# Optimization experiments

Hardware: AMD Instinct MI355X
Metric: run time of the kernel (lower is better)

## Reference

```python
import math
import jax, jax.numpy as jnp
import numpy as np

B, SQ, SK, D, H = 4, 2048, 2048, 1024, 16
HD = D // H  # 64


def setup_inputs() -> dict:
    key = jax.random.key(0)
    k1, k2, k3, k4, k5 = jax.random.split(key, 5)
    scale = 1.0 / math.sqrt(D)
    return {
        "hidden_states": jax.random.normal(k1, (B, SQ, D), dtype=jnp.float32),
        "encoder_hidden_states": jax.random.normal(k2, (B, SK, D), dtype=jnp.float32),
        "Wq": jax.random.normal(k3, (D, D), dtype=jnp.float32) * scale,
        "Wk": jax.random.normal(k4, (D, D), dtype=jnp.float32) * scale,
        "Wv": jax.random.normal(k5, (D, D), dtype=jnp.float32) * scale,
    }


def reference(hidden_states, encoder_hidden_states, Wq, Wk, Wv):
    # Linear (bias=False): y = x @ W^T, then split heads -> [B, H, S, HD]
    def split_heads(x, S):
        return x.reshape(B, S, H, HD).transpose(0, 2, 1, 3)

    q = split_heads(hidden_states @ Wq.T, SQ)
    k = split_heads(encoder_hidden_states @ Wk.T, SK)
    v = split_heads(encoder_hidden_states @ Wv.T, SK)

    scores = jnp.einsum("bhqd,bhkd->bhqk", q, k) / math.sqrt(HD)
    probs = jax.nn.softmax(scores, axis=-1)  # no mask, dropout p=0
    ctx = jnp.einsum("bhqk,bhkd->bhqd", probs, v)
    # merge heads -> [B, SQ, D]
    return ctx.transpose(0, 2, 1, 3).reshape(B, SQ, D)
```

## Files before the change

kernel.cpp:

```cpp
#include <hip/hip_runtime.h>
#include <hip/hip_bf16.h>

typedef unsigned short u16;
typedef unsigned int u32;
typedef __attribute__((ext_vector_type(8))) short bf16x8;
typedef __attribute__((ext_vector_type(4))) float f32x4;

#define MFMA32(a, b, c) __builtin_amdgcn_mfma_f32_16x16x32_bf16(a, b, c, 0, 0, 0)

__device__ __forceinline__ float fexp2(float x) { return __builtin_amdgcn_exp2f(x); }

__device__ __forceinline__ u16 f2bf(float f) {
  u32 u = __float_as_uint(f);
  u += 0x7fffu + ((u >> 16) & 1u);
  return (u16)(u >> 16);
}
__device__ __forceinline__ u32 pack2rn(float a, float b) {
  return (u32)f2bf(a) | ((u32)f2bf(b) << 16);
}
__device__ __forceinline__ bf16x8 cvt8(const float4 a, const float4 b) {
  union { bf16x8 v; u32 p[4]; } r;
  r.p[0] = pack2rn(a.x, a.y); r.p[1] = pack2rn(a.z, a.w);
  r.p[2] = pack2rn(b.x, b.y); r.p[3] = pack2rn(b.z, b.w);
  return r.v;
}

__device__ __forceinline__ u32 cvtpk(float lo, float hi) {
  u32 r;
  asm("v_cvt_pk_bf16_f32 %0, %1, %2" : "=v"(r) : "v"(lo), "v"(hi));
  return r;
}
__device__ __forceinline__ void pl32swap(u32& a, u32& b) {
  asm("v_permlane32_swap_b32 %0, %1" : "+v"(a), "+v"(b));
}
__device__ __forceinline__ void pl16swap(u32& a, u32& b) {
  asm("v_permlane16_swap_b32 %0, %1" : "+v"(a), "+v"(b));
}

__device__ __forceinline__ void async_copy16(const void* g, void* l) {
  __builtin_amdgcn_global_load_lds(
      (const __attribute__((address_space(1))) unsigned int*)g,
      (__attribute__((address_space(3))) unsigned int*)l, 16, 0, 0);
}

__global__ __launch_bounds__(256) void cvt_bf16(
    const float* __restrict__ s0, const float* __restrict__ s1,
    const float* __restrict__ s2, const float* __restrict__ s3,
    const float* __restrict__ s4,
    u16* __restrict__ d0, u16* __restrict__ d1, u16* __restrict__ d2,
    u16* __restrict__ d3, u16* __restrict__ d4) {
  const int z = blockIdx.z;
  const float* s = (z == 0) ? s0 : (z == 1) ? s1 : (z == 2) ? s2 : (z == 3) ? s3 : s4;
  u16* d = (z == 0) ? d0 : (z == 1) ? d1 : (z == 2) ? d2 : (z == 3) ? d3 : d4;
  const int n8 = ((z < 2) ? (8192 * 1024) : (1024 * 1024)) / 8;
  const int stride = gridDim.x * 256;
  for (int i = blockIdx.x * 256 + threadIdx.x; i < n8; i += stride) {
    const float4 a = *(const float4*)(s + (size_t)i * 8);
    const float4 b = *(const float4*)(s + (size_t)i * 8 + 4);
    *(bf16x8*)(d + (size_t)i * 8) = cvt8(a, b);
  }
}

__global__ __launch_bounds__(256) void proj_gemm_bf(
    const u16* __restrict__ hb, const u16* __restrict__ eb,
    const u16* __restrict__ wb,
    u16* __restrict__ qb, u16* __restrict__ kb, u16* __restrict__ vt) {
  const int z = blockIdx.z;
  const u16* Ag = (z == 0) ? hb : eb;
  const u16* Bg = wb + (size_t)z * 1024 * 1024;
  const int m0 = blockIdx.y * 128;
  const int n0 = blockIdx.x * 128;
  __shared__ __attribute__((aligned(16))) u16 Al[128 * 32];
  __shared__ __attribute__((aligned(16))) u16 Bl[128 * 32];
  const int tid = threadIdx.x;
  const int w = tid >> 6, lane = tid & 63;
  const int wm = w >> 1, wn = w & 1;
  const int l15 = lane & 15, quad = lane >> 4;
  const int srow = lane >> 2, sch = lane & 3;

  f32x4 acc[4][4] = {};

  for (int k0 = 0; k0 < 1024; k0 += 32) {
    __syncthreads();
#pragma unroll
    for (int j = 0; j < 2; j++) {
      const int row = w * 32 + j * 16 + srow;
      async_copy16(Ag + (size_t)(m0 + row) * 1024 + k0 + sch * 8,
                   &Al[(w * 32 + j * 16) * 32]);
      async_copy16(Bg + (size_t)(n0 + row) * 1024 + k0 + sch * 8,
                   &Bl[(w * 32 + j * 16) * 32]);
    }
    __syncthreads();
    bf16x8 af[4], bfr[4];
#pragma unroll
    for (int t = 0; t < 4; t++) {
      af[t] = *(const bf16x8*)&Al[(wm * 64 + t * 16 + l15) * 32 + quad * 8];
      bfr[t] = *(const bf16x8*)&Bl[(wn * 64 + t * 16 + l15) * 32 + quad * 8];
    }
#pragma unroll
    for (int mt = 0; mt < 4; mt++)
#pragma unroll
      for (int nt = 0; nt < 4; nt++)
        acc[mt][nt] = MFMA32(af[mt], bfr[nt], acc[mt][nt]);
  }

  if (z < 2) {
    u16* C = (z == 0) ? qb : kb;
    const float sc = (z == 0) ? 0.18033688011112042f : 1.0f;
#pragma unroll
    for (int mt = 0; mt < 4; mt++)
#pragma unroll
      for (int nt = 0; nt < 4; nt++) {
        const int col = n0 + wn * 64 + nt * 16 + l15;
#pragma unroll
        for (int rr = 0; rr < 4; rr++) {
          const int rowm = m0 + wm * 64 + mt * 16 + quad * 4 + rr;
          C[(size_t)rowm * 1024 + col] = f2bf(acc[mt][nt][rr] * sc);
        }
      }
  } else {
    const int b = m0 >> 11;
#pragma unroll
    for (int mt = 0; mt < 4; mt++) {
      const int key = (m0 & 2047) + wm * 64 + mt * 16 + quad * 4;
#pragma unroll
      for (int nt = 0; nt < 4; nt++) {
        const int n = n0 + wn * 64 + nt * 16 + l15;
        const int h = n >> 6, hd = n & 63;
        uint2 v;
        v.x = pack2rn(acc[mt][nt][0], acc[mt][nt][1]);
        v.y = pack2rn(acc[mt][nt][2], acc[mt][nt][3]);
        *(uint2*)&vt[((size_t)((b * 16 + h) * 64 + hd)) * 2048 + key] = v;
      }
    }
  }
}

__global__ __launch_bounds__(256) void proj_gemm_f32(
    const float* __restrict__ hs, const float* __restrict__ ehs,
    const float* __restrict__ wq, const float* __restrict__ wk,
    const float* __restrict__ wv,
    u16* __restrict__ qb, u16* __restrict__ kb, u16* __restrict__ vt) {
  const int z = blockIdx.z;
  const float* Ag = (z == 0) ? hs : ehs;
  const float* Bg = (z == 0) ? wq : ((z == 1) ? wk : wv);
  const int m0 = blockIdx.y * 128;
  const int n0 = blockIdx.x * 128;
  __shared__ __attribute__((aligned(16))) u16 Al[128 * 40];
  __shared__ __attribute__((aligned(16))) u16 Bl[128 * 40];
  const int tid = threadIdx.x;
  const int w = tid >> 6, lane = tid & 63;
  const int wm = w >> 1, wn = w & 1;
  const int l15 = lane & 15, quad = lane >> 4;
  const int srow = lane >> 2, sch = lane & 3;
  const int r0 = w * 32 + srow, r1 = r0 + 16;

  const float* Ap0 = Ag + (size_t)(m0 + r0) * 1024 + sch * 8;
  const float* Ap1 = Ag + (size_t)(m0 + r1) * 1024 + sch * 8;
  const float* Bp0 = Bg + (size_t)(n0 + r0) * 1024 + sch * 8;
  const float* Bp1 = Bg + (size_t)(n0 + r1) * 1024 + sch * 8;

  f32x4 acc[4][4] = {};

  for (int k0 = 0; k0 < 1024; k0 += 32) {
    const float4 a0l = *(const float4*)(Ap0 + k0), a0h = *(const float4*)(Ap0 + k0 + 4);
    const float4 a1l = *(const float4*)(Ap1 + k0), a1h = *(const float4*)(Ap1 + k0 + 4);
    const float4 b0l = *(const float4*)(Bp0 + k0), b0h = *(const float4*)(Bp0 + k0 + 4);
    const float4 b1l = *(const float4*)(Bp1 + k0), b1h = *(const float4*)(Bp1 + k0 + 4);
    __syncthreads();
    *(bf16x8*)&Al[r0 * 40 + sch * 8] = cvt8(a0l, a0h);
    *(bf16x8*)&Al[r1 * 40 + sch * 8] = cvt8(a1l, a1h);
    *(bf16x8*)&Bl[r0 * 40 + sch * 8] = cvt8(b0l, b0h);
    *(bf16x8*)&Bl[r1 * 40 + sch * 8] = cvt8(b1l, b1h);
    __syncthreads();
    bf16x8 af[4], bfr[4];
#pragma unroll
    for (int t = 0; t < 4; t++) {
      af[t] = *(const bf16x8*)&Al[(wm * 64 + t * 16 + l15) * 40 + quad * 8];
      bfr[t] = *(const bf16x8*)&Bl[(wn * 64 + t * 16 + l15) * 40 + quad * 8];
    }
#pragma unroll
    for (int mt = 0; mt < 4; mt++)
#pragma unroll
      for (int nt = 0; nt < 4; nt++)
        acc[mt][nt] = MFMA32(af[mt], bfr[nt], acc[mt][nt]);
  }

  if (z < 2) {
    u16* C = (z == 0) ? qb : kb;
    const float sc = (z == 0) ? 0.18033688011112042f : 1.0f;
#pragma unroll
    for (int mt = 0; mt < 4; mt++)
#pragma unroll
      for (int nt = 0; nt < 4; nt++) {
        const int col = n0 + wn * 64 + nt * 16 + l15;
#pragma unroll
        for (int rr = 0; rr < 4; rr++) {
          const int rowm = m0 + wm * 64 + mt * 16 + quad * 4 + rr;
          C[(size_t)rowm * 1024 + col] = f2bf(acc[mt][nt][rr] * sc);
        }
      }
  } else {
    const int b = m0 >> 11;
#pragma unroll
    for (int mt = 0; mt < 4; mt++) {
      const int key = (m0 & 2047) + wm * 64 + mt * 16 + quad * 4;
#pragma unroll
      for (int nt = 0; nt < 4; nt++) {
        const int n = n0 + wn * 64 + nt * 16 + l15;
        const int h = n >> 6, hd = n & 63;
        uint2 v;
        v.x = pack2rn(acc[mt][nt][0], acc[mt][nt][1]);
        v.y = pack2rn(acc[mt][nt][2], acc[mt][nt][3]);
        *(uint2*)&vt[((size_t)((b * 16 + h) * 64 + hd)) * 2048 + key] = v;
      }
    }
  }
}

__global__ __launch_bounds__(256, 3) void attn_fwd(
    const u16* __restrict__ qb, const u16* __restrict__ kb,
    const u16* __restrict__ vt, float* __restrict__ out) {
  const int bh = blockIdx.y;
  const int b = bh >> 4, h = bh & 15;
  const int q0 = blockIdx.x * 128;
  const int tid = threadIdx.x;
  const int w = tid >> 6, lane = tid & 63;
  const int l15 = lane & 15, quad = lane >> 4;

  __shared__ __attribute__((aligned(16))) u16 Kl[64 * 64];
  __shared__ __attribute__((aligned(16))) u16 Vl[64 * 64];

  const int wq = w * 32;
  bf16x8 qf[2][2];
#pragma unroll
  for (int nt = 0; nt < 2; nt++)
#pragma unroll
    for (int ks = 0; ks < 2; ks++)
      qf[nt][ks] = *(const bf16x8*)&qb[((size_t)(b * 2048 + q0 + wq + nt * 16 + l15)) * 1024 +
                                       h * 64 + ks * 32 + quad * 8];

  f32x4 o[4][2] = {};
  float l_[2] = {0.f, 0.f};

  const int srow = tid >> 3, sch = tid & 7;
  const int swzst = (srow & 7) << 3;
  const int rsw = (l15 & 7) << 3;
  const u16* Kg = kb + ((size_t)b * 2048) * 1024 + h * 64;
  const u16* Vg = vt + ((size_t)((b * 16 + h) * 64)) * 2048;

  bf16x8 kv[2], vv[2];
#pragma unroll
  for (int j = 0; j < 2; j++) {
    const int row = srow + j * 32;
    kv[j] = *(const bf16x8*)&Kg[(size_t)row * 1024 + sch * 8];
    vv[j] = *(const bf16x8*)&Vg[(size_t)row * 2048 + sch * 8];
  }

  for (int kt0 = 0; kt0 < 2048; kt0 += 64) {
    __syncthreads();
#pragma unroll
    for (int j = 0; j < 2; j++) {
      const int row = srow + j * 32;
      *(bf16x8*)&Kl[row * 64 + ((sch * 8) ^ swzst)] = kv[j];
      *(bf16x8*)&Vl[row * 64 + ((sch * 8) ^ swzst)] = vv[j];
    }
    __syncthreads();

    const int ktn = (kt0 + 64) & 2047;
#pragma unroll
    for (int j = 0; j < 2; j++) {
      const int row = srow + j * 32;
      kv[j] = *(const bf16x8*)&Kg[(size_t)(ktn + row) * 1024 + sch * 8];
      vv[j] = *(const bf16x8*)&Vg[(size_t)row * 2048 + ktn + sch * 8];
    }

    f32x4 s[4][2];
#pragma unroll
    for (int mt = 0; mt < 4; mt++)
#pragma unroll
      for (int nt = 0; nt < 2; nt++)
        s[mt][nt] = (f32x4){-16.f, -16.f, -16.f, -16.f};
#pragma unroll
    for (int mt = 0; mt < 4; mt++)
#pragma unroll
      for (int ks = 0; ks < 2; ks++) {
        const bf16x8 kf =
            *(const bf16x8*)&Kl[(mt * 16 + l15) * 64 + ((ks * 32 + quad * 8) ^ rsw)];
#pragma unroll
        for (int nt = 0; nt < 2; nt++)
          s[mt][nt] = MFMA32(kf, qf[nt][ks], s[mt][nt]);
      }

#pragma unroll
    for (int nt = 0; nt < 2; nt++) {
      float sum = 0.f;
#pragma unroll
      for (int mt = 0; mt < 4; mt++)
#pragma unroll
        for (int rr = 0; rr < 4; rr++) {
          const float p = fexp2(s[mt][nt][rr]);
          s[mt][nt][rr] = p;
          sum += p;
        }
      l_[nt] += sum;
    }

#pragma unroll
    for (int kt = 0; kt < 2; kt++) {
      bf16x8 pf[2];
#pragma unroll
      for (int nt = 0; nt < 2; nt++) {
        u32 r00 = cvtpk(s[2 * kt][nt][0], s[2 * kt][nt][1]);
        u32 r01 = cvtpk(s[2 * kt][nt][2], s[2 * kt][nt][3]);
        u32 r10 = cvtpk(s[2 * kt + 1][nt][0], s[2 * kt + 1][nt][1]);
        u32 r11 = cvtpk(s[2 * kt + 1][nt][2], s[2 * kt + 1][nt][3]);
        pl32swap(r00, r10);
        pl32swap(r01, r11);
        pl16swap(r00, r10);
        pl16swap(r01, r11);
        union { bf16x8 v; u32 p[4]; } u;
        u.p[0] = r00; u.p[1] = r01; u.p[2] = r10; u.p[3] = r11;
        pf[nt] = u.v;
      }
#pragma unroll
      for (int ht = 0; ht < 4; ht++) {
        const bf16x8 vf =
            *(const bf16x8*)&Vl[(ht * 16 + l15) * 64 + ((kt * 32 + quad * 8) ^ rsw)];
        o[ht][0] = MFMA32(vf, pf[0], o[ht][0]);
        o[ht][1] = MFMA32(vf, pf[1], o[ht][1]);
      }
    }
  }

#pragma unroll
  for (int nt = 0; nt < 2; nt++) {
    float ls = l_[nt];
    ls += __shfl_xor(ls, 16);
    ls += __shfl_xor(ls, 32);
    const float rl = 1.0f / ls;
    const size_t rowOff = ((size_t)(b * 2048 + q0 + wq + nt * 16 + l15)) * 1024 + h * 64;
#pragma unroll
    for (int ht = 0; ht < 4; ht++) {
      float4 v;
      v.x = o[ht][nt][0] * rl;
      v.y = o[ht][nt][1] * rl;
      v.z = o[ht][nt][2] * rl;
      v.w = o[ht][nt][3] * rl;
      *(float4*)&out[rowOff + ht * 16 + quad * 4] = v;
    }
  }
}

extern "C" void kernel_launch(void* const* d_in, const int* in_sizes, int n_in,
                              void* d_out, int out_size, void* d_ws, size_t ws_size,
                              hipStream_t stream) {
  const float* hs  = (const float*)d_in[0];
  const float* ehs = (const float*)d_in[1];
  const float* wqp = (const float*)d_in[2];
  const float* wkp = (const float*)d_in[3];
  const float* wvp = (const float*)d_in[4];
  const size_t M8 = (size_t)8192 * 1024;
  u16* qb = (u16*)d_ws;
  u16* kb = qb + M8;
  u16* vt = kb + M8;
  float* ob = (float*)d_out;

  const size_t need = (3 * M8 + 2 * M8 + 3 * (size_t)1024 * 1024) * 2;
  if (ws_size >= need) {
    u16* hb = vt + M8;
    u16* eb = hb + M8;
    u16* wb = eb + M8;
    dim3 gc(512, 1, 5);
    cvt_bf16<<<gc, dim3(256), 0, stream>>>(hs, ehs, wqp, wkp, wvp,
                                           hb, eb, wb, wb + M8 / 8, wb + M8 / 4);
    dim3 gg(8, 64, 3);
    proj_gemm_bf<<<gg, dim3(256), 0, stream>>>(hb, eb, wb, qb, kb, vt);
  } else {
    dim3 gg(8, 64, 3);
    proj_gemm_f32<<<gg, dim3(256), 0, stream>>>(hs, ehs, wqp, wkp, wvp, qb, kb, vt);
  }
  dim3 ga(16, 64, 1);
  attn_fwd<<<ga, dim3(256), 0, stream>>>(qb, kb, vt, ob);
}
```

Before: 276.5 us.

## Double-buffer K/V tiles with async global-to-LDS copies and MFMA row sums

```diff
diff --git a/kernel.cpp b/kernel.cpp
--- a/kernel.cpp
+++ b/kernel.cpp
@@ -228,8 +228,8 @@
   const int w = tid >> 6, lane = tid & 63;
   const int l15 = lane & 15, quad = lane >> 4;
 
-  __shared__ __attribute__((aligned(16))) u16 Kl[64 * 64];
-  __shared__ __attribute__((aligned(16))) u16 Vl[64 * 64];
+  __shared__ __attribute__((aligned(16))) u16 Kl[2][64 * 64];
+  __shared__ __attribute__((aligned(16))) u16 Vl[2][64 * 64];
 
   const int wq = w * 32;
   bf16x8 qf[2][2];
@@ -241,70 +241,62 @@
                                        h * 64 + ks * 32 + quad * 8];
 
   f32x4 o[4][2] = {};
-  float l_[2] = {0.f, 0.f};
-
-  const int srow = tid >> 3, sch = tid & 7;
-  const int swzst = (srow & 7) << 3;
+  f32x4 lacc[2] = {};
+  const f32x4 z4 = {0.f, 0.f, 0.f, 0.f};
+  union { bf16x8 v; u32 p[4]; } one_;
+  one_.p[0] = one_.p[1] = one_.p[2] = one_.p[3] = 0x3F803F80u;
+  const bf16x8 ones = one_.v;
+
   const int rsw = (l15 & 7) << 3;
-  const u16* Kg = kb + ((size_t)b * 2048) * 1024 + h * 64;
-  const u16* Vg = vt + ((size_t)((b * 16 + h) * 64)) * 2048;
-
-  bf16x8 kv[2], vv[2];
+  const int lr = lane >> 3;
+  const int cs8 = ((lane & 7) ^ lr) * 8;
+  const u16* Kp = kb + ((size_t)(b * 2048 + w * 16 + lr)) * 1024 + h * 64 + cs8;
+  const u16* Vp = vt + ((size_t)((b * 16 + h) * 64 + w * 16 + lr)) * 2048 + cs8;
+
 #pragma unroll
   for (int j = 0; j < 2; j++) {
-    const int row = srow + j * 32;
-    kv[j] = *(const bf16x8*)&Kg[(size_t)row * 1024 + sch * 8];
-    vv[j] = *(const bf16x8*)&Vg[(size_t)row * 2048 + sch * 8];
-  }
-
-  for (int kt0 = 0; kt0 < 2048; kt0 += 64) {
-    __syncthreads();
-#pragma unroll
-    for (int j = 0; j < 2; j++) {
-      const int row = srow + j * 32;
-      *(bf16x8*)&Kl[row * 64 + ((sch * 8) ^ swzst)] = kv[j];
-      *(bf16x8*)&Vl[row * 64 + ((sch * 8) ^ swzst)] = vv[j];
-    }
-    __syncthreads();
-
-    const int ktn = (kt0 + 64) & 2047;
-#pragma unroll
-    for (int j = 0; j < 2; j++) {
-      const int row = srow + j * 32;
-      kv[j] = *(const bf16x8*)&Kg[(size_t)(ktn + row) * 1024 + sch * 8];
-      vv[j] = *(const bf16x8*)&Vg[(size_t)row * 2048 + ktn + sch * 8];
-    }
+    async_copy16(Kp + (size_t)j * 8 * 1024, &Kl[0][(w * 16 + j * 8) * 64]);
+    async_copy16(Vp + (size_t)j * 8 * 2048, &Vl[0][(w * 16 + j * 8) * 64]);
+  }
+
+  for (int t = 0; t < 32; ++t) {
+    const int cur = t & 1;
+    __syncthreads();
+    if (t < 31) {
+      const size_t ko = (size_t)(t + 1) * 64;
+#pragma unroll
+      for (int j = 0; j < 2; j++) {
+        async_copy16(Kp + (ko + (size_t)j * 8) * 1024,
+                     &Kl[cur ^ 1][(w * 16 + j * 8) * 64]);
+        async_copy16(Vp + (size_t)j * 8 * 2048 + ko,
+                     &Vl[cur ^ 1][(w * 16 + j * 8) * 64]);
+      }
+    }
+    const u16* Kc = Kl[cur];
+    const u16* Vc = Vl[cur];
 
     f32x4 s[4][2];
 #pragma unroll
+    for (int mt = 0; mt < 4; mt++) {
+      const bf16x8 kf = *(const bf16x8*)&Kc[(mt * 16 + l15) * 64 + ((quad * 8) ^ rsw)];
+      s[mt][0] = MFMA32(kf, qf[0][0], z4);
+      s[mt][1] = MFMA32(kf, qf[1][0], z4);
+    }
+#pragma unroll
+    for (int mt = 0; mt < 4; mt++) {
+      const bf16x8 kf =
+          *(const bf16x8*)&Kc[(mt * 16 + l15) * 64 + ((32 + quad * 8) ^ rsw)];
+      s[mt][0] = MFMA32(kf, qf[0][1], s[mt][0]);
+      s[mt][1] = MFMA32(kf, qf[1][1], s[mt][1]);
+    }
+
+#pragma unroll
     for (int mt = 0; mt < 4; mt++)
 #pragma unroll
       for (int nt = 0; nt < 2; nt++)
-        s[mt][nt] = (f32x4){-16.f, -16.f, -16.f, -16.f};
-#pragma unroll
-    for (int mt = 0; mt < 4; mt++)
-#pragma unroll
-      for (int ks = 0; ks < 2; ks++) {
-        const bf16x8 kf =
-            *(const bf16x8*)&Kl[(mt * 16 + l15) * 64 + ((ks * 32 + quad * 8) ^ rsw)];
-#pragma unroll
-        for (int nt = 0; nt < 2; nt++)
-          s[mt][nt] = MFMA32(kf, qf[nt][ks], s[mt][nt]);
-      }
-
-#pragma unroll
-    for (int nt = 0; nt < 2; nt++) {
-      float sum = 0.f;
-#pragma unroll
-      for (int mt = 0; mt < 4; mt++)
-#pragma unroll
-        for (int rr = 0; rr < 4; rr++) {
-          const float p = fexp2(s[mt][nt][rr]);
-          s[mt][nt][rr] = p;
-          sum += p;
-        }
-      l_[nt] += sum;
-    }
+#pragma unroll
+        for (int rr = 0; rr < 4; rr++)
+          s[mt][nt][rr] = fexp2(s[mt][nt][rr]);
 
 #pragma unroll
     for (int kt = 0; kt < 2; kt++) {
@@ -323,10 +315,12 @@
         u.p[0] = r00; u.p[1] = r01; u.p[2] = r10; u.p[3] = r11;
         pf[nt] = u.v;
       }
+      lacc[0] = MFMA32(ones, pf[0], lacc[0]);
+      lacc[1] = MFMA32(ones, pf[1], lacc[1]);
 #pragma unroll
       for (int ht = 0; ht < 4; ht++) {
         const bf16x8 vf =
-            *(const bf16x8*)&Vl[(ht * 16 + l15) * 64 + ((kt * 32 + quad * 8) ^ rsw)];
+            *(const bf16x8*)&Vc[(ht * 16 + l15) * 64 + ((kt * 32 + quad * 8) ^ rsw)];
         o[ht][0] = MFMA32(vf, pf[0], o[ht][0]);
         o[ht][1] = MFMA32(vf, pf[1], o[ht][1]);
       }
@@ -335,10 +329,7 @@
 
 #pragma unroll
   for (int nt = 0; nt < 2; nt++) {
-    float ls = l_[nt];
-    ls += __shfl_xor(ls, 16);
-    ls += __shfl_xor(ls, 32);
-    const float rl = 1.0f / ls;
+    const float rl = 1.0f / lacc[nt][0];
     const size_t rowOff = ((size_t)(b * 2048 + q0 + wq + nt * 16 + l15)) * 1024 + h * 64;
 #pragma unroll
     for (int ht = 0; ht < 4; ht++) {
```

After: 277.3 us. No clear change (+0.3%).
